# Performance work log

Measured on AMD Instinct MI355X. Metric: run time of the kernel, lower is better.

The kernel has to match this reference:

```python
import jax, jax.numpy as jnp
from jax import lax
import numpy as np

V, D_EMB, H, P, B, T = 32000, 512, 1024, 512, 32, 512
NUM_LAYERS = 2


def setup_inputs() -> dict:
    key = jax.random.key(0)
    ks = jax.random.split(key, 2 + NUM_LAYERS * 5)
    tokens = jax.random.randint(ks[0], (B, T), 0, V, dtype=jnp.int32)
    embed = jax.random.normal(ks[1], (V, D_EMB), dtype=jnp.float32) * 0.02
    inp = {"tokens": tokens, "embed": embed}
    in_dims = [D_EMB] + [P] * (NUM_LAYERS - 1)
    for l in range(NUM_LAYERS):
        kk = ks[2 + 5 * l: 7 + 5 * l]
        inp[f"Wx{l}"] = jax.random.normal(kk[0], (in_dims[l], 4 * H), dtype=jnp.float32) * 0.02
        inp[f"Wh{l}"] = jax.random.normal(kk[1], (H, 4 * H), dtype=jnp.float32) * 0.02
        inp[f"b{l}"] = jnp.zeros((4 * H,), dtype=jnp.float32)
        inp[f"Wfc{l}"] = jax.random.normal(kk[3], (H, P), dtype=jnp.float32) * 0.02
        inp[f"bfc{l}"] = jnp.zeros((P,), dtype=jnp.float32)
    return inp


def _lstm(x, Wx, Wh, b):
    # x: [B, T, D] -> [B, T, H]. Keras gate order: i, f, g(cell), o.
    Bsz = x.shape[0]
    h0 = jnp.zeros((Bsz, H), dtype=x.dtype)
    c0 = jnp.zeros((Bsz, H), dtype=x.dtype)

    # Precompute input projection for all timesteps (one big GEMM).
    xz = jnp.einsum('btd,dg->btg', x, Wx) + b  # [B, T, 4H]

    def step(carry, zt):
        h, c = carry
        z = zt + h @ Wh
        i, f, g, o = jnp.split(z, 4, axis=-1)
        c = jax.nn.sigmoid(f) * c + jax.nn.sigmoid(i) * jnp.tanh(g)
        h = jax.nn.sigmoid(o) * jnp.tanh(c)
        return (h, c), h

    _, ys = lax.scan(step, (h0, c0), jnp.swapaxes(xz, 0, 1))  # ys: [T, B, H]
    return jnp.swapaxes(ys, 0, 1)


def reference(tokens, embed, Wx0, Wh0, b0, Wfc0, bfc0, Wx1, Wh1, b1, Wfc1, bfc1):
    # inference path: dropout is identity (training=False), use_softmax=False
    x = embed[tokens]  # [B, T, D_EMB]
    layers = [(Wx0, Wh0, b0, Wfc0, bfc0), (Wx1, Wh1, b1, Wfc1, bfc1)]
    for Wx, Wh, b, Wfc, bfc in layers:
        x = _lstm(x, Wx, Wh, b)
        x = x @ Wfc + bfc  # per-layer dense projection [B, T, P]
    return x
```

## Files before the change

### kernel.cpp

```cpp
#include <hip/hip_runtime.h>
#include <cstdio>
#include <cstdint>

typedef unsigned short u16;
typedef unsigned int u32;
typedef float f32x4 __attribute__((ext_vector_type(4)));
typedef short s16x8 __attribute__((ext_vector_type(8)));
typedef int i32x2 __attribute__((ext_vector_type(2)));

#define DI __device__ __forceinline__

#define BATCH 32
#define SEQT 512
#define HDIM 1024
#define PDIM 512
#define DEMB 512
#define G4H 4096

DI u16 f2bf(float f) {
  u32 u = __float_as_uint(f);
  return (u16)((u + 0x7fffu + ((u >> 16) & 1u)) >> 16);
}
DI float bf2f(u16 h) { return __uint_as_float(((u32)h) << 16); }
DI void split2(float f, u16 &hi, u16 &lo) {
  hi = f2bf(f);
  lo = f2bf(f - bf2f(hi));
}
DI f32x4 mfma16(s16x8 a, s16x8 b, f32x4 c) {
  return __builtin_amdgcn_mfma_f32_16x16x32_bf16(a, b, c, 0, 0, 0);
}
DI void dma16(const void *g, void *l) {
  __builtin_amdgcn_global_load_lds((const __attribute__((address_space(1))) void *)g,
                                   (__attribute__((address_space(3))) void *)l, 16, 0, 0);
}
DI s16x8 ld128_dev(const u16 *p) {
  s16x8 r;
  asm volatile("global_load_dwordx4 %0, %1, off sc1" : "=v"(r) : "v"(p));
  return r;
}
DI i32x2 ld64_dev(const u16 *p) {
  i32x2 r;
  asm volatile("global_load_dwordx2 %0, %1, off sc1" : "=v"(r) : "v"(p));
  return r;
}
DI void st16_dev(u16 *p, u16 v) {
  asm volatile("global_store_short %0, %1, off sc1" ::"v"(p), "v"((u32)v) : "memory");
}
DI void st32_dev(int *p, int v) {
  asm volatile("global_store_dword %0, %1, off sc1" ::"v"(p), "v"(v) : "memory");
}
DI void st64_dev(u16 *p, i32x2 v) {
  asm volatile("global_store_dwordx2 %0, %1, off sc1" ::"v"(p), "v"(v) : "memory");
}

#if __has_builtin(__builtin_amdgcn_exp2f) && __has_builtin(__builtin_amdgcn_rcpf)
DI float fsig(float x) {
  return __builtin_amdgcn_rcpf(1.f + __builtin_amdgcn_exp2f(-1.4426950408889634f * x));
}
DI float ftanh(float x) {
  return 2.f * __builtin_amdgcn_rcpf(1.f + __builtin_amdgcn_exp2f(-2.8853900817779268f * x)) - 1.f;
}
#else
DI float fsig(float x) { return 1.f / (1.f + expf(-x)); }
DI float ftanh(float x) { return tanhf(x); }
#endif

__global__ void k_gather_pack(const int *__restrict__ tokens, const float *__restrict__ embed,
                              u16 *__restrict__ xhi, u16 *__restrict__ xlo) {
  int idx = blockIdx.x * 256 + threadIdx.x;
  int m = idx >> 6;
  int k8 = (idx & 63) << 3;
  int tok = tokens[m];
  const float *src = embed + (size_t)tok * DEMB + k8;
  float4 a = *(const float4 *)src;
  float4 b = *(const float4 *)(src + 4);
  float v[8] = {a.x, a.y, a.z, a.w, b.x, b.y, b.z, b.w};
  union UV { u16 h[8]; int4 v; };
  UV uh, ul;
#pragma unroll
  for (int j = 0; j < 8; ++j) split2(v[j], uh.h[j], ul.h[j]);
  size_t o = (size_t)m * DEMB + k8;
  *(int4 *)(xhi + o) = uh.v;
  *(int4 *)(xlo + o) = ul.v;
}

__global__ void k_packT(const float *__restrict__ W, u16 *__restrict__ Thi, u16 *__restrict__ Tlo,
                        int K, int N) {
  __shared__ float tile[32][33];
  int n0 = blockIdx.x * 32, k0 = blockIdx.y * 32;
  int tx = threadIdx.x, ty = threadIdx.y;
#pragma unroll
  for (int i = 0; i < 4; ++i) tile[ty + 8 * i][tx] = W[(size_t)(k0 + ty + 8 * i) * N + n0 + tx];
  __syncthreads();
#pragma unroll
  for (int i = 0; i < 4; ++i) {
    int n = ty + 8 * i;
    u16 hi, lo;
    split2(tile[tx][n], hi, lo);
    size_t o = (size_t)(n0 + n) * K + k0 + tx;
    Thi[o] = hi;
    Tlo[o] = lo;
  }
}

__global__ void k_split(const float *__restrict__ W, u16 *__restrict__ hi, u16 *__restrict__ lo,
                        int n) {
  int i = blockIdx.x * 256 + threadIdx.x;
  if (i < n) split2(W[i], hi[i], lo[i]);
}

__global__ void k_beff(const float *__restrict__ bfc0, const float *__restrict__ Wx1,
                       const float *__restrict__ b1, float *__restrict__ beff) {
  int n = blockIdx.x * 256 + threadIdx.x;
  float acc = b1[n];
  for (int j = 0; j < PDIM; ++j) acc += bfc0[j] * Wx1[(size_t)j * G4H + n];
  beff[n] = acc;
}

template <int OM, int SA>
__global__ __launch_bounds__(256, 2) void k_gemm(const u16 *__restrict__ Ahi, const u16 *__restrict__ Alo,
                                                 const u16 *__restrict__ Bhi, const u16 *__restrict__ Blo,
                                                 const float *__restrict__ bias, void *__restrict__ out0,
                                                 int M, int N, int K) {
  __shared__ u16 sP[4][128 * 64];
  const int tid = threadIdx.x;
  const int w = tid >> 6, lane = tid & 63;
  const int la15 = lane & 15, la4 = lane >> 4;
  const int nbn = N >> 7;
  const int bm = blockIdx.x / nbn, bn = blockIdx.x % nbn;
  const u16 *src = (w == 0) ? Ahi : (w == 1) ? Alo : (w == 2) ? Bhi : Blo;
  const int rowbase = (w < 2) ? bm * 128 : bn * 128;
  char *lds = (char *)&sP[w][0];

  if (SA) {
    for (int i = tid; i < 2048; i += 256) ((unsigned long long *)&sP[1][0])[i] = 0ULL;
  }

  f32x4 acc[2][8] = {};
  for (int kb = 0; kb < K; kb += 64) {
    if (!(SA && w == 1)) {
#pragma unroll
      for (int i = 0; i < 16; ++i) {
        int s = i * 64 + lane;
        int row = s >> 3;
        int k16 = (s & 7) ^ (row & 7);
        dma16(src + (size_t)(rowbase + row) * K + kb + k16 * 8, lds + i * 1024);
      }
    }
    asm volatile("s_waitcnt vmcnt(0)" ::: "memory");
    __syncthreads();
#pragma unroll
    for (int ksl = 0; ksl < 2; ++ksl) {
      s16x8 ah[2], al[2];
#pragma unroll
      for (int rf = 0; rf < 2; ++rf) {
        int row = 32 * w + 16 * rf + la15;
        int slot = row * 8 + ((4 * ksl + la4) ^ (row & 7));
        ah[rf] = *(const s16x8 *)((const char *)&sP[0][0] + slot * 16);
        al[rf] = *(const s16x8 *)((const char *)&sP[1][0] + slot * 16);
      }
#pragma unroll
      for (int cf = 0; cf < 8; ++cf) {
        int col = 16 * cf + la15;
        int slot = col * 8 + ((4 * ksl + la4) ^ (col & 7));
        s16x8 bh = *(const s16x8 *)((const char *)&sP[2][0] + slot * 16);
        s16x8 bl = *(const s16x8 *)((const char *)&sP[3][0] + slot * 16);
#pragma unroll
        for (int rf = 0; rf < 2; ++rf) {
          acc[rf][cf] = mfma16(ah[rf], bh, acc[rf][cf]);
          acc[rf][cf] = mfma16(ah[rf], bl, acc[rf][cf]);
          acc[rf][cf] = mfma16(al[rf], bh, acc[rf][cf]);
        }
      }
    }
    __syncthreads();
  }
#pragma unroll
  for (int rf = 0; rf < 2; ++rf) {
#pragma unroll
    for (int cf = 0; cf < 8; ++cf) {
      int c = bn * 128 + 16 * cf + la15;
      float bv = bias ? bias[c] : 0.f;
#pragma unroll
      for (int q = 0; q < 4; ++q) {
        int r = bm * 128 + 32 * w + 16 * rf + 4 * la4 + q;
        float v = acc[rf][cf][q] + bv;
        if (OM == 0) {
          ((u16 *)out0)[(size_t)r * N + c] = f2bf(v);
        } else {
          int b2 = r & 31, tt = r >> 5;
          ((float *)out0)[((size_t)b2 * SEQT + tt) * PDIM + c] = v;
        }
      }
    }
  }
}

__global__ __launch_bounds__(256, 1) void k_recur_pipe(
    const u16 *__restrict__ xz0, const float *__restrict__ Wh0, const float *__restrict__ Wh1,
    const u16 *__restrict__ Weff, const float *__restrict__ beff,
    u16 *h0h, u16 *h1h, u16 *zeffR, int *flags) {
  __shared__ u16 sW[32 * 1024];
  __shared__ u16 sE[32 * 1024];
  __shared__ float zacc[4][32][33];
  __shared__ float sC[256];
  const int tid = threadIdx.x;
  const int w = tid >> 6, lane = tid & 63;
  const int la15 = lane & 15, la4 = lane >> 4;
  const int wg = blockIdx.x;
  const int layer = wg >> 7;
  const int g = wg & 127;

  const float *Wh = layer ? Wh1 : Wh0;
  for (int i2 = tid; i2 < 32 * 1024; i2 += 256) {
    int zc = i2 & 31;
    int k = i2 >> 5;
    int gcol = (zc >> 3) * HDIM + 8 * g + (zc & 7);
    int boff = zc * 2048 + ((((k >> 3) ^ (zc & 7))) << 4) + (k & 7) * 2;
    *(u16 *)((char *)sW + boff) = f2bf(Wh[(size_t)k * G4H + gcol]);
    if (!layer) *(u16 *)((char *)sE + boff) = Weff[(size_t)k * G4H + gcol];
  }
  sC[tid] = 0.f;
  __syncthreads();

  const int r_g = tid >> 3, hc = tid & 7;
  const int ks0 = 8 * w;

  if (!layer) {
    for (int t = 0; t <= SEQT; ++t) {
      const bool last = (t == SEQT);
      float xzv[4] = {0.f, 0.f, 0.f, 0.f};
      if (!last) {
        const u16 *px = xz0 + ((size_t)r_g * SEQT + t) * G4H + 8 * g + hc;
#pragma unroll
        for (int gi = 0; gi < 4; ++gi) xzv[gi] = bf2f(px[(size_t)gi * HDIM]);
      }
      if (w == 0 && t > 0) {
        const int *f0 = flags + lane;
        const int *f1 = flags + 128 + lane;
        const int bp = t - 16;
        for (long tries = 0;; ++tries) {
          int a = __hip_atomic_load(f0, __ATOMIC_RELAXED, __HIP_MEMORY_SCOPE_AGENT);
          int b = __hip_atomic_load(f0 + 64, __ATOMIC_RELAXED, __HIP_MEMORY_SCOPE_AGENT);
          bool ok = (a >= t && b >= t);
          if (t > 16) {
            int c = __hip_atomic_load(f1, __ATOMIC_RELAXED, __HIP_MEMORY_SCOPE_AGENT);
            int d = __hip_atomic_load(f1 + 64, __ATOMIC_RELAXED, __HIP_MEMORY_SCOPE_AGENT);
            ok = ok && (c >= bp && d >= bp);
          }
          if (__all(ok)) break;
          if (tries > (1L << 22)) break;
          __builtin_amdgcn_s_sleep(1);
        }
      }
      __syncthreads();
      f32x4 accE[2][2] = {};
      if (t > 0) {
        const u16 *pA = h0h + (size_t)(t - 1) * 32 * HDIM;
        s16x8 aw0[8], aw1[8];
#pragma unroll
        for (int j8 = 0; j8 < 8; ++j8)
          aw0[j8] = ld128_dev(pA + (size_t)la15 * HDIM + 32 * (ks0 + j8) + 8 * la4);
#pragma unroll
        for (int j8 = 0; j8 < 8; ++j8)
          aw1[j8] = ld128_dev(pA + (size_t)(16 + la15) * HDIM + 32 * (ks0 + j8) + 8 * la4);
        asm volatile("s_waitcnt vmcnt(0)" ::: "memory");
        __builtin_amdgcn_sched_barrier(0);
        {
          f32x4 acc0[2] = {};
#pragma unroll
          for (int j8 = 0; j8 < 8; ++j8) {
#pragma unroll
            for (int cf = 0; cf < 2; ++cf) {
              int zc = 16 * cf + la15;
              int sl = (4 * (ks0 + j8) + la4) ^ (zc & 7);
              int boff = zc * 2048 + (sl << 4);
              if (!last) acc0[cf] = mfma16(aw0[j8], *(const s16x8 *)((const char *)sW + boff), acc0[cf]);
              accE[0][cf] = mfma16(aw0[j8], *(const s16x8 *)((const char *)sE + boff), accE[0][cf]);
            }
          }
          if (!last) {
#pragma unroll
            for (int cf = 0; cf < 2; ++cf)
#pragma unroll
              for (int q = 0; q < 4; ++q) zacc[w][4 * la4 + q][16 * cf + la15] = acc0[cf][q];
          }
        }
        {
          f32x4 acc0[2] = {};
#pragma unroll
          for (int j8 = 0; j8 < 8; ++j8) {
#pragma unroll
            for (int cf = 0; cf < 2; ++cf) {
              int zc = 16 * cf + la15;
              int sl = (4 * (ks0 + j8) + la4) ^ (zc & 7);
              int boff = zc * 2048 + (sl << 4);
              if (!last) acc0[cf] = mfma16(aw1[j8], *(const s16x8 *)((const char *)sW + boff), acc0[cf]);
              accE[1][cf] = mfma16(aw1[j8], *(const s16x8 *)((const char *)sE + boff), accE[1][cf]);
            }
          }
          if (!last) {
#pragma unroll
            for (int cf = 0; cf < 2; ++cf)
#pragma unroll
              for (int q = 0; q < 4; ++q) zacc[w][16 + 4 * la4 + q][16 * cf + la15] = acc0[cf][q];
          }
        }
      }
      __syncthreads();
      if (!last) {
        float z4[4];
#pragma unroll
        for (int gi = 0; gi < 4; ++gi) {
          float s = xzv[gi];
          if (t > 0) {
            int zc = gi * 8 + hc;
            s += zacc[0][r_g][zc] + zacc[1][r_g][zc] + zacc[2][r_g][zc] + zacc[3][r_g][zc];
          }
          z4[gi] = s;
        }
        float ig = fsig(z4[0]);
        float fg = fsig(z4[1]);
        float gg = ftanh(z4[2]);
        float og = fsig(z4[3]);
        float c = fg * sC[tid] + ig * gg;
        sC[tid] = c;
        float h = og * ftanh(c);
        st16_dev(h0h + ((size_t)t * 32 + r_g) * HDIM + 8 * g + hc, f2bf(h));
      }
      __syncthreads();
      if (t > 0) {
#pragma unroll
        for (int rt = 0; rt < 2; ++rt)
#pragma unroll
          for (int cf = 0; cf < 2; ++cf)
#pragma unroll
            for (int q = 0; q < 4; ++q)
              zacc[w][16 * rt + 4 * la4 + q][16 * cf + la15] = accE[rt][cf][q];
      }
      __syncthreads();
      if (t > 0) {
        float ze[4];
#pragma unroll
        for (int gi = 0; gi < 4; ++gi) {
          int zc = gi * 8 + hc;
          ze[gi] = zacc[0][r_g][zc] + zacc[1][r_g][zc] + zacc[2][r_g][zc] + zacc[3][r_g][zc];
        }
        i32x2 pk;
        pk[0] = (int)(((u32)f2bf(ze[1]) << 16) | (u32)f2bf(ze[0]));
        pk[1] = (int)(((u32)f2bf(ze[3]) << 16) | (u32)f2bf(ze[2]));
        st64_dev(zeffR + (((size_t)((t - 1) & 15) * 128 + g) << 10) + tid * 4, pk);
      }
      asm volatile("s_waitcnt vmcnt(0)" ::: "memory");
      __syncthreads();
      if (tid == 0) st32_dev(flags + g, t + 1);
    }
  } else {
    float bef[4];
#pragma unroll
    for (int gi = 0; gi < 4; ++gi) bef[gi] = beff[gi * HDIM + 8 * g + hc];
    for (int t = 0; t < SEQT; ++t) {
      if (w == 0) {
        const int *f0 = flags + lane;
        const int *f1 = flags + 128 + lane;
        const int need0 = t + 2;
        for (long tries = 0;; ++tries) {
          int a = __hip_atomic_load(f0, __ATOMIC_RELAXED, __HIP_MEMORY_SCOPE_AGENT);
          int b = __hip_atomic_load(f0 + 64, __ATOMIC_RELAXED, __HIP_MEMORY_SCOPE_AGENT);
          bool ok = (a >= need0 && b >= need0);
          if (t > 0) {
            int c = __hip_atomic_load(f1, __ATOMIC_RELAXED, __HIP_MEMORY_SCOPE_AGENT);
            int d = __hip_atomic_load(f1 + 64, __ATOMIC_RELAXED, __HIP_MEMORY_SCOPE_AGENT);
            ok = ok && (c >= t && d >= t);
          }
          if (__all(ok)) break;
          if (tries > (1L << 22)) break;
          __builtin_amdgcn_s_sleep(1);
        }
      }
      __syncthreads();
      s16x8 aw0[8], aw1[8];
      const u16 *pA = h1h + (size_t)(t - 1) * 32 * HDIM;
      if (t > 0) {
#pragma unroll
        for (int j8 = 0; j8 < 8; ++j8)
          aw0[j8] = ld128_dev(pA + (size_t)la15 * HDIM + 32 * (ks0 + j8) + 8 * la4);
#pragma unroll
        for (int j8 = 0; j8 < 8; ++j8)
          aw1[j8] = ld128_dev(pA + (size_t)(16 + la15) * HDIM + 32 * (ks0 + j8) + 8 * la4);
      }
      i32x2 zpk = ld64_dev(zeffR + (((size_t)(t & 15) * 128 + g) << 10) + tid * 4);
      asm volatile("s_waitcnt vmcnt(0)" ::: "memory");
      __builtin_amdgcn_sched_barrier(0);
      float zv[4];
      zv[0] = bf2f((u16)((u32)zpk[0] & 0xffffu));
      zv[1] = bf2f((u16)((u32)zpk[0] >> 16));
      zv[2] = bf2f((u16)((u32)zpk[1] & 0xffffu));
      zv[3] = bf2f((u16)((u32)zpk[1] >> 16));
      if (t > 0) {
        {
          f32x4 acc0[2] = {};
#pragma unroll
          for (int j8 = 0; j8 < 8; ++j8) {
#pragma unroll
            for (int cf = 0; cf < 2; ++cf) {
              int zc = 16 * cf + la15;
              int sl = (4 * (ks0 + j8) + la4) ^ (zc & 7);
              int boff = zc * 2048 + (sl << 4);
              acc0[cf] = mfma16(aw0[j8], *(const s16x8 *)((const char *)sW + boff), acc0[cf]);
            }
          }
#pragma unroll
          for (int cf = 0; cf < 2; ++cf)
#pragma unroll
            for (int q = 0; q < 4; ++q) zacc[w][4 * la4 + q][16 * cf + la15] = acc0[cf][q];
        }
        {
          f32x4 acc0[2] = {};
#pragma unroll
          for (int j8 = 0; j8 < 8; ++j8) {
#pragma unroll
            for (int cf = 0; cf < 2; ++cf) {
              int zc = 16 * cf + la15;
              int sl = (4 * (ks0 + j8) + la4) ^ (zc & 7);
              int boff = zc * 2048 + (sl << 4);
              acc0[cf] = mfma16(aw1[j8], *(const s16x8 *)((const char *)sW + boff), acc0[cf]);
            }
          }
#pragma unroll
          for (int cf = 0; cf < 2; ++cf)
#pragma unroll
            for (int q = 0; q < 4; ++q) zacc[w][16 + 4 * la4 + q][16 * cf + la15] = acc0[cf][q];
        }
      }
      __syncthreads();
      {
        float z4[4];
#pragma unroll
        for (int gi = 0; gi < 4; ++gi) {
          float s = bef[gi] + zv[gi];
          if (t > 0) {
            int zc = gi * 8 + hc;
            s += zacc[0][r_g][zc] + zacc[1][r_g][zc] + zacc[2][r_g][zc] + zacc[3][r_g][zc];
          }
          z4[gi] = s;
        }
        float ig = fsig(z4[0]);
        float fg = fsig(z4[1]);
        float gg = ftanh(z4[2]);
        float og = fsig(z4[3]);
        float c = fg * sC[tid] + ig * gg;
        sC[tid] = c;
        float h = og * ftanh(c);
        st16_dev(h1h + ((size_t)t * 32 + r_g) * HDIM + 8 * g + hc, f2bf(h));
      }
      asm volatile("s_waitcnt vmcnt(0)" ::: "memory");
      __syncthreads();
      if (tid == 0) st32_dev(flags + 128 + g, t + 1);
    }
  }
}

extern "C" void kernel_launch(void *const *d_in, const int *in_sizes, int n_in,
                              void *d_out, int out_size, void *d_ws, size_t ws_size,
                              hipStream_t stream) {
  const int *tokens = (const int *)d_in[0];
  const float *embed = (const float *)d_in[1];
  const float *Wx0 = (const float *)d_in[2];
  const float *Wh0 = (const float *)d_in[3];
  const float *b0 = (const float *)d_in[4];
  const float *Wfc0 = (const float *)d_in[5];
  const float *bfc0 = (const float *)d_in[6];
  const float *Wx1 = (const float *)d_in[7];
  const float *Wh1 = (const float *)d_in[8];
  const float *b1 = (const float *)d_in[9];
  const float *Wfc1 = (const float *)d_in[10];
  const float *bfc1 = (const float *)d_in[11];

  constexpr size_t NEED = 255856640;
  if (ws_size < NEED) {
    fprintf(stderr, "RNNLM kernel: ws too small (%zu < %zu)\n", ws_size, NEED);
    return;
  }
  char *ws = (char *)d_ws;
  u16 *xz0 = (u16 *)(ws + 0);
  u16 *h0h = (u16 *)(ws + 134217728);
  u16 *h1h = (u16 *)(ws + 167772160);
  u16 *x0hi = (u16 *)(ws + 201326592);
  u16 *x0lo = (u16 *)(ws + 218103808);
  u16 *Weff = (u16 *)(ws + 201326592);
  u16 *Wfc0hi = (u16 *)(ws + 209715200);
  u16 *Wfc0lo = (u16 *)(ws + 210763776);
  u16 *WfcT1hi = (u16 *)(ws + 211812352);
  u16 *WfcT1lo = (u16 *)(ws + 212860928);
  float *beff = (float *)(ws + 213909504);
  int *flags = (int *)(ws + 213925888);
  u16 *zeffR = (u16 *)(ws + 218103808);
  u16 *WxT0hi = (u16 *)(ws + 234881024);
  u16 *WxT0lo = (u16 *)(ws + 239075328);
  u16 *WxT1hi = (u16 *)(ws + 243269632);
  u16 *WxT1lo = (u16 *)(ws + 247463936);

  k_packT<<<dim3(G4H / 32, DEMB / 32), dim3(32, 8), 0, stream>>>(Wx0, WxT0hi, WxT0lo, DEMB, G4H);
  k_packT<<<dim3(G4H / 32, DEMB / 32), dim3(32, 8), 0, stream>>>(Wx1, WxT1hi, WxT1lo, DEMB, G4H);
  k_gather_pack<<<4096, 256, 0, stream>>>(tokens, embed, x0hi, x0lo);
  k_gemm<0, 0><<<dim3(128 * 32), 256, 0, stream>>>(x0hi, x0lo, WxT0hi, WxT0lo, b0, xz0,
                                                   16384, G4H, DEMB);
  k_split<<<2048, 256, 0, stream>>>(Wfc0, Wfc0hi, Wfc0lo, HDIM * PDIM);
  k_packT<<<dim3(PDIM / 32, HDIM / 32), dim3(32, 8), 0, stream>>>(Wfc1, WfcT1hi, WfcT1lo, HDIM, PDIM);
  k_beff<<<16, 256, 0, stream>>>(bfc0, Wx1, b1, beff);
  (void)hipMemsetAsync(flags, 0, 256 * sizeof(int), stream);
  k_gemm<0, 0><<<dim3(8 * 32), 256, 0, stream>>>(Wfc0hi, Wfc0lo, WxT1hi, WxT1lo, nullptr, Weff,
                                                 1024, G4H, PDIM);
  {
    const u16 *a0 = xz0; const float *a1 = Wh0; const float *a2 = Wh1;
    const u16 *a3 = Weff; const float *a4 = beff;
    u16 *a5 = h0h; u16 *a6 = h1h; u16 *a7 = zeffR; int *a8 = flags;
    void *args[] = {&a0, &a1, &a2, &a3, &a4, &a5, &a6, &a7, &a8};
    hipError_t e = hipLaunchCooperativeKernel((void *)k_recur_pipe, dim3(256), dim3(256), args, 0, stream);
    if (e != hipSuccess) fprintf(stderr, "coop launch failed: %d\n", (int)e);
  }
  k_gemm<2, 1><<<dim3(128 * 4), 256, 0, stream>>>(h1h, h1h, WfcT1hi, WfcT1lo, bfc1, d_out,
                                                  16384, PDIM, HDIM);
}
```

Before: 5.151 ms.

## Replace per-step flag barriers with sentinel-based data polling in recurrent pipeline

```diff
diff --git a/kernel.cpp b/kernel.cpp
--- a/kernel.cpp
+++ b/kernel.cpp
@@ -51,6 +51,15 @@
 }
 DI void st64_dev(u16 *p, i32x2 v) {
   asm volatile("global_store_dwordx2 %0, %1, off sc1" ::"v"(p), "v"(v) : "memory");
+}
+DI u32 sentq(s16x8 v) {
+  union U { s16x8 s; u32 d[4]; } u;
+  u.s = v;
+  u32 b = 0;
+#pragma unroll
+  for (int i = 0; i < 4; ++i)
+    b |= (u32)(((u.d[i] & 0xffffu) == 0xffffu) || ((u.d[i] >> 16) == 0xffffu));
+  return b;
 }
 
 #if __has_builtin(__builtin_amdgcn_exp2f) && __has_builtin(__builtin_amdgcn_rcpf)
@@ -235,37 +244,37 @@
 #pragma unroll
         for (int gi = 0; gi < 4; ++gi) xzv[gi] = bf2f(px[(size_t)gi * HDIM]);
       }
-      if (w == 0 && t > 0) {
-        const int *f0 = flags + lane;
+      if (w == 0 && (t & 7) == 0 && t >= 26) {
         const int *f1 = flags + 128 + lane;
-        const int bp = t - 16;
+        const int bp = t - 25;
         for (long tries = 0;; ++tries) {
-          int a = __hip_atomic_load(f0, __ATOMIC_RELAXED, __HIP_MEMORY_SCOPE_AGENT);
-          int b = __hip_atomic_load(f0 + 64, __ATOMIC_RELAXED, __HIP_MEMORY_SCOPE_AGENT);
-          bool ok = (a >= t && b >= t);
-          if (t > 16) {
-            int c = __hip_atomic_load(f1, __ATOMIC_RELAXED, __HIP_MEMORY_SCOPE_AGENT);
-            int d = __hip_atomic_load(f1 + 64, __ATOMIC_RELAXED, __HIP_MEMORY_SCOPE_AGENT);
-            ok = ok && (c >= bp && d >= bp);
-          }
-          if (__all(ok)) break;
+          int c = __hip_atomic_load(f1, __ATOMIC_RELAXED, __HIP_MEMORY_SCOPE_AGENT);
+          int d = __hip_atomic_load(f1 + 64, __ATOMIC_RELAXED, __HIP_MEMORY_SCOPE_AGENT);
+          if (__all(c >= bp && d >= bp)) break;
           if (tries > (1L << 22)) break;
           __builtin_amdgcn_s_sleep(1);
         }
       }
-      __syncthreads();
       f32x4 accE[2][2] = {};
       if (t > 0) {
         const u16 *pA = h0h + (size_t)(t - 1) * 32 * HDIM;
         s16x8 aw0[8], aw1[8];
-#pragma unroll
-        for (int j8 = 0; j8 < 8; ++j8)
-          aw0[j8] = ld128_dev(pA + (size_t)la15 * HDIM + 32 * (ks0 + j8) + 8 * la4);
-#pragma unroll
-        for (int j8 = 0; j8 < 8; ++j8)
-          aw1[j8] = ld128_dev(pA + (size_t)(16 + la15) * HDIM + 32 * (ks0 + j8) + 8 * la4);
-        asm volatile("s_waitcnt vmcnt(0)" ::: "memory");
-        __builtin_amdgcn_sched_barrier(0);
+        for (long tries = 0;; ++tries) {
+#pragma unroll
+          for (int j8 = 0; j8 < 8; ++j8)
+            aw0[j8] = ld128_dev(pA + (size_t)la15 * HDIM + 32 * (ks0 + j8) + 8 * la4);
+#pragma unroll
+          for (int j8 = 0; j8 < 8; ++j8)
+            aw1[j8] = ld128_dev(pA + (size_t)(16 + la15) * HDIM + 32 * (ks0 + j8) + 8 * la4);
+          asm volatile("s_waitcnt vmcnt(0)" ::: "memory");
+          __builtin_amdgcn_sched_barrier(0);
+          u32 bad = 0;
+#pragma unroll
+          for (int j8 = 0; j8 < 8; ++j8) bad |= sentq(aw0[j8]) | sentq(aw1[j8]);
+          if (__all(bad == 0)) break;
+          if (tries > (1L << 17)) break;
+          __builtin_amdgcn_s_sleep(2);
+        }
         {
           f32x4 acc0[2] = {};
 #pragma unroll
@@ -349,7 +358,7 @@
         i32x2 pk;
         pk[0] = (int)(((u32)f2bf(ze[1]) << 16) | (u32)f2bf(ze[0]));
         pk[1] = (int)(((u32)f2bf(ze[3]) << 16) | (u32)f2bf(ze[2]));
-        st64_dev(zeffR + (((size_t)((t - 1) & 15) * 128 + g) << 10) + tid * 4, pk);
+        st64_dev(zeffR + (((size_t)((t - 1) & 31) * 128 + g) << 10) + tid * 4, pk);
       }
       asm volatile("s_waitcnt vmcnt(0)" ::: "memory");
       __syncthreads();
@@ -360,36 +369,28 @@
 #pragma unroll
     for (int gi = 0; gi < 4; ++gi) bef[gi] = beff[gi * HDIM + 8 * g + hc];
     for (int t = 0; t < SEQT; ++t) {
-      if (w == 0) {
+      s16x8 aw0[8], aw1[8];
+      const u16 *pA = h1h + ((t > 0) ? (size_t)(t - 1) * 32 * HDIM : 0);
+      if (t > 0) {
+#pragma unroll
+        for (int j8 = 0; j8 < 8; ++j8)
+          aw0[j8] = ld128_dev(pA + (size_t)la15 * HDIM + 32 * (ks0 + j8) + 8 * la4);
+#pragma unroll
+        for (int j8 = 0; j8 < 8; ++j8)
+          aw1[j8] = ld128_dev(pA + (size_t)(16 + la15) * HDIM + 32 * (ks0 + j8) + 8 * la4);
+      }
+      {
         const int *f0 = flags + lane;
-        const int *f1 = flags + 128 + lane;
         const int need0 = t + 2;
         for (long tries = 0;; ++tries) {
           int a = __hip_atomic_load(f0, __ATOMIC_RELAXED, __HIP_MEMORY_SCOPE_AGENT);
           int b = __hip_atomic_load(f0 + 64, __ATOMIC_RELAXED, __HIP_MEMORY_SCOPE_AGENT);
-          bool ok = (a >= need0 && b >= need0);
-          if (t > 0) {
-            int c = __hip_atomic_load(f1, __ATOMIC_RELAXED, __HIP_MEMORY_SCOPE_AGENT);
-            int d = __hip_atomic_load(f1 + 64, __ATOMIC_RELAXED, __HIP_MEMORY_SCOPE_AGENT);
-            ok = ok && (c >= t && d >= t);
-          }
-          if (__all(ok)) break;
+          if (__all(a >= need0 && b >= need0)) break;
           if (tries > (1L << 22)) break;
           __builtin_amdgcn_s_sleep(1);
         }
       }
-      __syncthreads();
-      s16x8 aw0[8], aw1[8];
-      const u16 *pA = h1h + (size_t)(t - 1) * 32 * HDIM;
-      if (t > 0) {
-#pragma unroll
-        for (int j8 = 0; j8 < 8; ++j8)
-          aw0[j8] = ld128_dev(pA + (size_t)la15 * HDIM + 32 * (ks0 + j8) + 8 * la4);
-#pragma unroll
-        for (int j8 = 0; j8 < 8; ++j8)
-          aw1[j8] = ld128_dev(pA + (size_t)(16 + la15) * HDIM + 32 * (ks0 + j8) + 8 * la4);
-      }
-      i32x2 zpk = ld64_dev(zeffR + (((size_t)(t & 15) * 128 + g) << 10) + tid * 4);
+      i32x2 zpk = ld64_dev(zeffR + (((size_t)(t & 31) * 128 + g) << 10) + tid * 4);
       asm volatile("s_waitcnt vmcnt(0)" ::: "memory");
       __builtin_amdgcn_sched_barrier(0);
       float zv[4];
@@ -398,6 +399,22 @@
       zv[2] = bf2f((u16)((u32)zpk[1] & 0xffffu));
       zv[3] = bf2f((u16)((u32)zpk[1] >> 16));
       if (t > 0) {
+        for (long tries = 0;; ++tries) {
+          u32 bad = 0;
+#pragma unroll
+          for (int j8 = 0; j8 < 8; ++j8) bad |= sentq(aw0[j8]) | sentq(aw1[j8]);
+          if (__all(bad == 0)) break;
+          if (tries > (1L << 17)) break;
+          __builtin_amdgcn_s_sleep(2);
+#pragma unroll
+          for (int j8 = 0; j8 < 8; ++j8)
+            aw0[j8] = ld128_dev(pA + (size_t)la15 * HDIM + 32 * (ks0 + j8) + 8 * la4);
+#pragma unroll
+          for (int j8 = 0; j8 < 8; ++j8)
+            aw1[j8] = ld128_dev(pA + (size_t)(16 + la15) * HDIM + 32 * (ks0 + j8) + 8 * la4);
+          asm volatile("s_waitcnt vmcnt(0)" ::: "memory");
+          __builtin_amdgcn_sched_barrier(0);
+        }
         {
           f32x4 acc0[2] = {};
 #pragma unroll
@@ -434,6 +451,7 @@
         }
       }
       __syncthreads();
+      if (tid == 0) st32_dev(flags + 128 + g, t + 1);
       {
         float z4[4];
 #pragma unroll
@@ -454,9 +472,7 @@
         float h = og * ftanh(c);
         st16_dev(h1h + ((size_t)t * 32 + r_g) * HDIM + 8 * g + hc, f2bf(h));
       }
-      asm volatile("s_waitcnt vmcnt(0)" ::: "memory");
       __syncthreads();
-      if (tid == 0) st32_dev(flags + 128 + g, t + 1);
     }
   }
 }
@@ -501,6 +517,8 @@
   u16 *WxT1hi = (u16 *)(ws + 243269632);
   u16 *WxT1lo = (u16 *)(ws + 247463936);
 
+  (void)hipMemsetAsync(h0h, 0xFF, 67108864, stream);
+
   k_packT<<<dim3(G4H / 32, DEMB / 32), dim3(32, 8), 0, stream>>>(Wx0, WxT0hi, WxT0lo, DEMB, G4H);
   k_packT<<<dim3(G4H / 32, DEMB / 32), dim3(32, 8), 0, stream>>>(Wx1, WxT1hi, WxT1lo, DEMB, G4H);
   k_gather_pack<<<4096, 256, 0, stream>>>(tokens, embed, x0hi, x0lo);
```

After: 4.916 ms. 1.05x faster.
